# Performance work log

Hardware: AMD Instinct MI355X
Metric: run time of the kernel (lower is better)

Reference implementation:

```python
import jax, jax.numpy as jnp
import numpy as np

K_H, K_W = 3, 3
STRIDE, PAD = 1, 1
GN_GROUPS = 32
EPS = 1e-5


def setup_inputs() -> dict:
    key = jax.random.key(0)
    k1, k2, k3 = jax.random.split(key, 3)
    B, C, H, W = 4, 256, 64, 64
    Cout = 256
    x = jax.random.normal(k1, (B, C, H, W), jnp.float32)
    offset = jax.random.normal(k2, (B, 2 * K_H * K_W, H, W), jnp.float32)
    weight = jax.random.normal(k3, (Cout, C, K_H, K_W), jnp.float32) * 0.02
    gamma = jnp.ones((Cout,), jnp.float32)
    beta = jnp.zeros((Cout,), jnp.float32)
    return {"x": x, "offset": offset, "weight": weight, "gamma": gamma, "beta": beta}


def _deform_conv(x, offset, weight):
    B, C, H, W = x.shape
    Cout = weight.shape[0]
    K = K_H * K_W
    Ho = (H + 2 * PAD - K_H) // STRIDE + 1
    Wo = (W + 2 * PAD - K_W) // STRIDE + 1
    ky, kx = jnp.meshgrid(jnp.arange(K_H), jnp.arange(K_W), indexing='ij')
    ky = ky.reshape(K).astype(x.dtype)
    kx = kx.reshape(K).astype(x.dtype)
    # base sampling positions per kernel tap
    py_base = (jnp.arange(Ho) * STRIDE - PAD).astype(x.dtype)[None, :] + ky[:, None]  # [K,Ho]
    px_base = (jnp.arange(Wo) * STRIDE - PAD).astype(x.dtype)[None, :] + kx[:, None]  # [K,Wo]
    off = offset.reshape(B, K, 2, Ho, Wo)  # mmcv layout: (dy, dx) pairs per tap
    py = py_base[None, :, :, None] + off[:, :, 0]  # [B,K,Ho,Wo]
    px = px_base[None, :, None, :] + off[:, :, 1]  # [B,K,Ho,Wo]
    y0 = jnp.floor(py)
    x0 = jnp.floor(px)
    ly = py - y0
    lx = px - x0
    xf = x.reshape(B, C, H * W)

    def gather(yi, xi):
        valid = (yi >= 0) & (yi <= H - 1) & (xi >= 0) & (xi <= W - 1)
        yc = jnp.clip(yi, 0, H - 1).astype(jnp.int32)
        xc = jnp.clip(xi, 0, W - 1).astype(jnp.int32)
        idx = yc * W + xc  # [B,K,Ho,Wo]
        vals = jax.vmap(lambda xb, ib: xb[:, ib])(xf, idx)  # [B,C,K,Ho,Wo]
        return vals * valid[:, None].astype(x.dtype)

    g00 = gather(y0, x0)
    g01 = gather(y0, x0 + 1)
    g10 = gather(y0 + 1, x0)
    g11 = gather(y0 + 1, x0 + 1)
    wy = ly[:, None]  # [B,1,K,Ho,Wo]
    wx = lx[:, None]
    val = ((1 - wy) * (1 - wx) * g00 + (1 - wy) * wx * g01
           + wy * (1 - wx) * g10 + wy * wx * g11)  # [B,C,K,Ho,Wo]
    return jnp.einsum('bckhw,ock->bohw', val, weight.reshape(Cout, C, K))


def reference(x, offset, weight, gamma, beta):
    y = _deform_conv(x, offset, weight)  # [B,Cout,Ho,Wo]
    B, C, H, W = y.shape
    yg = y.reshape(B, GN_GROUPS, C // GN_GROUPS, H, W)
    mean = jnp.mean(yg, axis=(2, 3, 4), keepdims=True)
    var = jnp.var(yg, axis=(2, 3, 4), keepdims=True)
    yn = ((yg - mean) * jax.lax.rsqrt(var + EPS)).reshape(B, C, H, W)
    out = yn * gamma[None, :, None, None] + beta[None, :, None, None]
    return jax.nn.relu(out)
```

## Files before the change

### kernel.cpp

```cpp
#include <hip/hip_runtime.h>

typedef unsigned short ushort_t;
typedef __bf16 bf16x8 __attribute__((ext_vector_type(8)));
typedef float f32x4 __attribute__((ext_vector_type(4)));
typedef void __attribute__((address_space(1))) gvoid_t;
typedef void __attribute__((address_space(3))) lvoid_t;

__device__ __forceinline__ float bflo(unsigned u) { return __builtin_bit_cast(float, u << 16); }
__device__ __forceinline__ float bfhi(unsigned u) { return __builtin_bit_cast(float, u & 0xffff0000u); }
__device__ __forceinline__ unsigned f2bf_bits(float f) {
  unsigned u = __builtin_bit_cast(unsigned, f);
  return (u + 0x7fffu + ((u >> 16) & 1u)) >> 16;
}
__device__ __forceinline__ ushort_t f2bf(float f) { return (ushort_t)f2bf_bits(f); }

#define VMWAIT(N) asm volatile("s_waitcnt vmcnt(" #N ")" ::: "memory")
#define LGKM0 asm volatile("s_waitcnt lgkmcnt(0)" ::: "memory")

__global__ __launch_bounds__(256) void k_prep_w(const float* __restrict__ w,
                                                ushort_t* __restrict__ wb) {
  const int idx = blockIdx.x * 256 + threadIdx.x;
  const float* src = w + (size_t)idx * 9;
  #pragma unroll
  for (int k = 0; k < 9; ++k)
    wb[(k << 16) + idx] = f2bf(src[k]);
}

__global__ __launch_bounds__(256) void k_prep_x(const float* __restrict__ x,
                                                ushort_t* __restrict__ xt) {
  __shared__ ushort_t tile[64][68];
  const int bid = blockIdx.x;
  const int b = bid >> 8;
  const int ct = (bid >> 6) & 3;
  const int pt = bid & 63;
  const int t = threadIdx.x;
  const float* xb = x + ((size_t)(b * 256 + ct * 64)) * 4096 + pt * 64;
  #pragma unroll
  for (int i = 0; i < 16; ++i) {
    const int idx = t + 256 * i;
    const int c_l = idx >> 6, p_l = idx & 63;
    tile[c_l][p_l] = f2bf(xb[(size_t)c_l * 4096 + p_l]);
  }
  __syncthreads();
  ushort_t* xo = xt + ((size_t)(b * 4096 + pt * 64)) * 256 + ct * 64;
  #pragma unroll
  for (int i = 0; i < 16; ++i) {
    const int idx = t + 256 * i;
    const int p_l = idx >> 6, c_l = idx & 63;
    xo[(size_t)p_l * 256 + c_l] = tile[c_l][p_l];
  }
}

struct SMeta {
  float w00, w01, w10, w11;
  int i00, i01, i10, i11;
};
__device__ __forceinline__ SMeta meta_for(int h, int gw, int k, float oy, float ox) {
  SMeta m;
  const float py = (float)(h - 1 + k / 3) + oy;
  const float px = (float)(gw - 1 + k % 3) + ox;
  const float fy = floorf(py), fx = floorf(px);
  const float ly = py - fy, lx = px - fx;
  const int iy0 = (int)fy, ix0 = (int)fx;
  const float vy0 = (iy0 >= 0 && iy0 < 64) ? 1.f : 0.f;
  const float vy1 = (iy0 >= -1 && iy0 < 63) ? 1.f : 0.f;
  const float vx0 = (ix0 >= 0 && ix0 < 64) ? 1.f : 0.f;
  const float vx1 = (ix0 >= -1 && ix0 < 63) ? 1.f : 0.f;
  m.w00 = (1.f - ly) * (1.f - lx) * vy0 * vx0;
  m.w01 = (1.f - ly) * lx * vy0 * vx1;
  m.w10 = ly * (1.f - lx) * vy1 * vx0;
  m.w11 = ly * lx * vy1 * vx1;
  const int cy0 = min(max(iy0, 0), 63), cy1 = min(max(iy0 + 1, 0), 63);
  const int cx0 = min(max(ix0, 0), 63), cx1 = min(max(ix0 + 1, 0), 63);
  m.i00 = (cy0 * 64 + cx0) * 256;
  m.i01 = (cy0 * 64 + cx1) * 256;
  m.i10 = (cy1 * 64 + cx0) * 256;
  m.i11 = (cy1 * 64 + cx1) * 256;
  return m;
}

__device__ __forceinline__ unsigned lerp_pack(unsigned a, unsigned b, unsigned c, unsigned d,
                                              float w00, float w01, float w10, float w11) {
  float lo = w00 * bflo(a) + w01 * bflo(b) + w10 * bflo(c) + w11 * bflo(d);
  float hi = w00 * bfhi(a) + w01 * bfhi(b) + w10 * bfhi(c) + w11 * bfhi(d);
  return f2bf_bits(lo) | (f2bf_bits(hi) << 16);
}

__global__ __launch_bounds__(512) void k_gemm(const float* __restrict__ off,
                                              const ushort_t* __restrict__ xt,
                                              const ushort_t* __restrict__ wb,
                                              float* __restrict__ y,
                                              float* __restrict__ stats) {
  __shared__ __attribute__((aligned(16))) ushort_t Abuf[2][2][64 * 64];
  __shared__ __attribute__((aligned(16))) ushort_t Bbuf[2][2][256 * 64];

  const int bid = blockIdx.x;
  const int lb = ((bid & 7) << 5) | (bid >> 3);
  const int b = lb >> 6;
  const int h = lb & 63;
  const int t = threadIdx.x;
  const int wave = t >> 6;
  const int lane = t & 63;
  const int wq = lane >> 4;
  const int wr = lane & 15;
  const int wm = wave >> 2;
  const int wn = wave & 3;

  const int s_w = t >> 3;
  const int c8 = t & 7;

  const f32x4 zero = {0.f, 0.f, 0.f, 0.f};
  f32x4 acc[2][4];
  #pragma unroll
  for (int i = 0; i < 2; ++i)
    #pragma unroll
    for (int j = 0; j < 4; ++j) acc[i][j] = zero;

  const ushort_t* xtb = xt + (size_t)b * 4096 * 256;

  float oy[9], ox[9];
  {
    const float* offb = off + (size_t)b * 18 * 4096 + h * 64 + s_w;
    #pragma unroll
    for (int k = 0; k < 9; ++k) {
      oy[k] = offb[(2 * k) * 4096];
      ox[k] = offb[(2 * k + 1) * 4096];
    }
  }

  SMeta mg;
  uint4 qa00, qa01, qa10, qa11;
  uint4 qb00, qb01, qb10, qb11;

#define GATHER_ISSUE(TAP, C0)                             \
  {                                                       \
    mg = meta_for(h, s_w, (TAP), oy[(TAP)], ox[(TAP)]);   \
    const int cc = (C0) + c8 * 8;                         \
    qa00 = *(const uint4*)(xtb + mg.i00 + cc);            \
    qa01 = *(const uint4*)(xtb + mg.i01 + cc);            \
    qa10 = *(const uint4*)(xtb + mg.i10 + cc);            \
    qa11 = *(const uint4*)(xtb + mg.i11 + cc);            \
    qb00 = *(const uint4*)(xtb + mg.i00 + cc + 64);       \
    qb01 = *(const uint4*)(xtb + mg.i01 + cc + 64);       \
    qb10 = *(const uint4*)(xtb + mg.i10 + cc + 64);       \
    qb11 = *(const uint4*)(xtb + mg.i11 + cc + 64);       \
  }

#define B_ISSUE(TAP, C0, PB)                                                                   \
  {                                                                                            \
    _Pragma("unroll") for (int ch_ = 0; ch_ < 2; ++ch_) {                                      \
      _Pragma("unroll") for (int i_ = 0; i_ < 4; ++i_) {                                       \
        const int idx_ = i_ * 512 + t;                                                         \
        const int row_ = idx_ >> 3, slot_ = idx_ & 7;                                          \
        const ushort_t* g_ =                                                                   \
            wb + ((TAP) << 16) + row_ * 256 + (C0) + ch_ * 64 + ((slot_ ^ (row_ & 7)) << 3);   \
        __builtin_amdgcn_global_load_lds((gvoid_t*)g_,                                         \
                                         (lvoid_t*)((char*)&Bbuf[(PB)][ch_][0] + idx_ * 16),   \
                                         16, 0, 0);                                            \
      }                                                                                        \
    }                                                                                          \
  }

#define A_WRITE(PB)                                                                  \
  {                                                                                  \
    uint4 r;                                                                         \
    r.x = lerp_pack(qa00.x, qa01.x, qa10.x, qa11.x, mg.w00, mg.w01, mg.w10, mg.w11); \
    r.y = lerp_pack(qa00.y, qa01.y, qa10.y, qa11.y, mg.w00, mg.w01, mg.w10, mg.w11); \
    r.z = lerp_pack(qa00.z, qa01.z, qa10.z, qa11.z, mg.w00, mg.w01, mg.w10, mg.w11); \
    r.w = lerp_pack(qa00.w, qa01.w, qa10.w, qa11.w, mg.w00, mg.w01, mg.w10, mg.w11); \
    *(uint4*)&Abuf[(PB)][0][s_w * 64 + ((c8 ^ (s_w & 7)) << 3)] = r;                 \
    r.x = lerp_pack(qb00.x, qb01.x, qb10.x, qb11.x, mg.w00, mg.w01, mg.w10, mg.w11); \
    r.y = lerp_pack(qb00.y, qb01.y, qb10.y, qb11.y, mg.w00, mg.w01, mg.w10, mg.w11); \
    r.z = lerp_pack(qb00.z, qb01.z, qb10.z, qb11.z, mg.w00, mg.w01, mg.w10, mg.w11); \
    r.w = lerp_pack(qb00.w, qb01.w, qb10.w, qb11.w, mg.w00, mg.w01, mg.w10, mg.w11); \
    *(uint4*)&Abuf[(PB)][1][s_w * 64 + ((c8 ^ (s_w & 7)) << 3)] = r;                 \
  }

  {
    GATHER_ISSUE(0, 0);
    B_ISSUE(0, 0, 0);
    A_WRITE(0);
    GATHER_ISSUE(0, 128);
    VMWAIT(8);
    LGKM0;
    __builtin_amdgcn_s_barrier();
  }

  #pragma unroll
  for (int p = 0; p < 18; ++p) {
    const int pb = p & 1;
    const int nb = pb ^ 1;
    if (p < 17) {
      const int tap1 = (p + 1) >> 1;
      const int c01 = ((p + 1) & 1) << 7;
      B_ISSUE(tap1, c01, nb);
    }
    #pragma unroll
    for (int ks = 0; ks < 4; ++ks) {
      const int ch = ks >> 1;
      const int kk = ks & 1;
      bf16x8 af[2], bfr[4];
      #pragma unroll
      for (int tm = 0; tm < 2; ++tm) {
        const int row = wm * 32 + tm * 16 + wr;
        const int slot = (kk * 4 + wq) ^ (row & 7);
        af[tm] = *(const bf16x8*)&Abuf[pb][ch][row * 64 + slot * 8];
      }
      #pragma unroll
      for (int tn = 0; tn < 4; ++tn) {
        const int row = wn * 64 + tn * 16 + wr;
        const int slot = (kk * 4 + wq) ^ (row & 7);
        bfr[tn] = *(const bf16x8*)&Bbuf[pb][ch][row * 64 + slot * 8];
      }
      #pragma unroll
      for (int tm = 0; tm < 2; ++tm)
        #pragma unroll
        for (int tn = 0; tn < 4; ++tn)
          acc[tm][tn] =
              __builtin_amdgcn_mfma_f32_16x16x32_bf16(af[tm], bfr[tn], acc[tm][tn], 0, 0, 0);
    }
    if (p < 17) {
      A_WRITE(nb);
      if (p < 16) {
        const int tap2 = (p + 2) >> 1;
        const int c02 = ((p + 2) & 1) << 7;
        GATHER_ISSUE(tap2, c02);
        VMWAIT(8);
      } else {
        VMWAIT(0);
      }
      LGKM0;
      __builtin_amdgcn_s_barrier();
    }
  }
#undef GATHER_ISSUE
#undef B_ISSUE
#undef A_WRITE

  float* yb = y + ((size_t)(b * 4096 + h * 64)) * 256;
  #pragma unroll
  for (int tm = 0; tm < 2; ++tm) {
    #pragma unroll
    for (int tn = 0; tn < 4; ++tn) {
      const int o = wn * 64 + tn * 16 + wr;
      #pragma unroll
      for (int r2 = 0; r2 < 4; ++r2) {
        const int ww = wm * 32 + tm * 16 + wq * 4 + r2;
        yb[ww * 256 + o] = acc[tm][tn][r2];
      }
    }
  }
  #pragma unroll
  for (int tn = 0; tn < 4; ++tn) {
    float sum = 0.f, ss = 0.f;
    #pragma unroll
    for (int tm = 0; tm < 2; ++tm)
      #pragma unroll
      for (int r2 = 0; r2 < 4; ++r2) {
        const float v = acc[tm][tn][r2];
        sum += v;
        ss += v * v;
      }
    sum += __shfl_xor(sum, 16, 64);
    ss += __shfl_xor(ss, 16, 64);
    sum += __shfl_xor(sum, 32, 64);
    ss += __shfl_xor(ss, 32, 64);
    #pragma unroll
    for (int d = 1; d < 8; d <<= 1) {
      sum += __shfl_xor(sum, d, 64);
      ss += __shfl_xor(ss, d, 64);
    }
    if (wq == 0 && (wr & 7) == 0) {
      const int gi = wn * 8 + tn * 2 + (wr >> 3);
      atomicAdd(&stats[(b * 32 + gi) * 2], sum);
      atomicAdd(&stats[(b * 32 + gi) * 2 + 1], ss);
    }
  }
}

__global__ __launch_bounds__(256) void k_apply(const float* __restrict__ y,
                                               const float* __restrict__ stats,
                                               const float* __restrict__ gamma,
                                               const float* __restrict__ beta,
                                               float* __restrict__ out) {
  __shared__ float tile[64][65];
  __shared__ float sm[8], sr[8], sg[64], sb[64];
  const int bid = blockIdx.x;
  const int lb = ((bid & 7) << 7) | (bid >> 3);
  const int b = lb >> 8;
  const int st = (lb >> 2) & 63;
  const int ot = lb & 3;
  const int t = threadIdx.x;
  if (t < 8) {
    const int g = ot * 8 + t;
    const float s1 = stats[(b * 32 + g) * 2];
    const float s2 = stats[(b * 32 + g) * 2 + 1];
    const float mean = s1 * (1.f / 32768.f);
    const float var = s2 * (1.f / 32768.f) - mean * mean;
    sm[t] = mean;
    sr[t] = rsqrtf(var + 1e-5f);
  }
  if (t < 64) {
    sg[t] = gamma[ot * 64 + t];
    sb[t] = beta[ot * 64 + t];
  }
  const float* yb = y + ((size_t)(b * 4096 + st * 64)) * 256 + ot * 64;
  #pragma unroll
  for (int i = 0; i < 16; ++i) {
    const int idx = t + 256 * i;
    const int s_l = idx >> 6, o_l = idx & 63;
    tile[s_l][o_l] = yb[(size_t)s_l * 256 + o_l];
  }
  __syncthreads();
  float* ob = out + ((size_t)(b * 256 + ot * 64)) * 4096 + st * 64;
  #pragma unroll
  for (int i = 0; i < 16; ++i) {
    const int idx = t + 256 * i;
    const int o_l = idx >> 6, s_l = idx & 63;
    const int g = o_l >> 3;
    float v = (tile[s_l][o_l] - sm[g]) * sr[g] * sg[o_l] + sb[o_l];
    v = v > 0.f ? v : 0.f;
    ob[(size_t)o_l * 4096 + s_l] = v;
  }
}

extern "C" void kernel_launch(void* const* d_in, const int* in_sizes, int n_in,
                              void* d_out, int out_size, void* d_ws, size_t ws_size,
                              hipStream_t stream) {
  const float* x = (const float*)d_in[0];
  const float* off = (const float*)d_in[1];
  const float* w = (const float*)d_in[2];
  const float* gamma = (const float*)d_in[3];
  const float* beta = (const float*)d_in[4];
  float* out = (float*)d_out;

  char* ws = (char*)d_ws;
  float* y = (float*)(ws);
  ushort_t* xt = (ushort_t*)(ws + 16777216);
  ushort_t* wb = (ushort_t*)(ws + 25165824);
  float* stats = (float*)(ws + 26345472);

  hipMemsetAsync(stats, 0, 1024, stream);
  k_prep_w<<<256, 256, 0, stream>>>(w, wb);
  k_prep_x<<<1024, 256, 0, stream>>>(x, xt);
  k_gemm<<<256, 512, 0, stream>>>(off, xt, wb, y, stats);
  k_apply<<<1024, 256, 0, stream>>>(y, stats, gamma, beta, out);
}
```

Baseline: 83.74 us.

## Split GEMM block into producer and consumer waves with warp specialization

```diff
diff --git a/kernel.cpp b/kernel.cpp
--- a/kernel.cpp
+++ b/kernel.cpp
@@ -103,23 +103,23 @@
   const int lane = t & 63;
   const int wq = lane >> 4;
   const int wr = lane & 15;
-  const int wm = wave >> 2;
+  const bool prod = (wave >= 4);
   const int wn = wave & 3;
-
-  const int s_w = t >> 3;
-  const int c8 = t & 7;
+  const int pt = t & 255;
+  const int s_w = pt >> 2;
+  const int c4 = pt & 3;
 
   const f32x4 zero = {0.f, 0.f, 0.f, 0.f};
-  f32x4 acc[2][4];
-  #pragma unroll
-  for (int i = 0; i < 2; ++i)
+  f32x4 acc[4][4];
+  #pragma unroll
+  for (int i = 0; i < 4; ++i)
     #pragma unroll
     for (int j = 0; j < 4; ++j) acc[i][j] = zero;
 
   const ushort_t* xtb = xt + (size_t)b * 4096 * 256;
 
   float oy[9], ox[9];
-  {
+  if (prod) {
     const float* offb = off + (size_t)b * 18 * 4096 + h * 64 + s_w;
     #pragma unroll
     for (int k = 0; k < 9; ++k) {
@@ -128,152 +128,139 @@
     }
   }
 
-  SMeta mg;
-  uint4 qa00, qa01, qa10, qa11;
-  uint4 qb00, qb01, qb10, qb11;
-
-#define GATHER_ISSUE(TAP, C0)                             \
-  {                                                       \
-    mg = meta_for(h, s_w, (TAP), oy[(TAP)], ox[(TAP)]);   \
-    const int cc = (C0) + c8 * 8;                         \
-    qa00 = *(const uint4*)(xtb + mg.i00 + cc);            \
-    qa01 = *(const uint4*)(xtb + mg.i01 + cc);            \
-    qa10 = *(const uint4*)(xtb + mg.i10 + cc);            \
-    qa11 = *(const uint4*)(xtb + mg.i11 + cc);            \
-    qb00 = *(const uint4*)(xtb + mg.i00 + cc + 64);       \
-    qb01 = *(const uint4*)(xtb + mg.i01 + cc + 64);       \
-    qb10 = *(const uint4*)(xtb + mg.i10 + cc + 64);       \
-    qb11 = *(const uint4*)(xtb + mg.i11 + cc + 64);       \
-  }
-
-#define B_ISSUE(TAP, C0, PB)                                                                   \
+#define STAGE(TAP, C0, PB)                                                                     \
   {                                                                                            \
+    const SMeta m = meta_for(h, s_w, (TAP), oy[(TAP)], ox[(TAP)]);                             \
+    uint4 g[2][2][4];                                                                          \
     _Pragma("unroll") for (int ch_ = 0; ch_ < 2; ++ch_) {                                      \
-      _Pragma("unroll") for (int i_ = 0; i_ < 4; ++i_) {                                       \
-        const int idx_ = i_ * 512 + t;                                                         \
-        const int row_ = idx_ >> 3, slot_ = idx_ & 7;                                          \
-        const ushort_t* g_ =                                                                   \
-            wb + ((TAP) << 16) + row_ * 256 + (C0) + ch_ * 64 + ((slot_ ^ (row_ & 7)) << 3);   \
-        __builtin_amdgcn_global_load_lds((gvoid_t*)g_,                                         \
-                                         (lvoid_t*)((char*)&Bbuf[(PB)][ch_][0] + idx_ * 16),   \
-                                         16, 0, 0);                                            \
+      _Pragma("unroll") for (int sg_ = 0; sg_ < 2; ++sg_) {                                    \
+        const int cc_ = (C0) + ch_ * 64 + (c4 + sg_ * 4) * 8;                                  \
+        g[ch_][sg_][0] = *(const uint4*)(xtb + m.i00 + cc_);                                   \
+        g[ch_][sg_][1] = *(const uint4*)(xtb + m.i01 + cc_);                                   \
+        g[ch_][sg_][2] = *(const uint4*)(xtb + m.i10 + cc_);                                   \
+        g[ch_][sg_][3] = *(const uint4*)(xtb + m.i11 + cc_);                                   \
       }                                                                                        \
     }                                                                                          \
-  }
-
-#define A_WRITE(PB)                                                                  \
-  {                                                                                  \
-    uint4 r;                                                                         \
-    r.x = lerp_pack(qa00.x, qa01.x, qa10.x, qa11.x, mg.w00, mg.w01, mg.w10, mg.w11); \
-    r.y = lerp_pack(qa00.y, qa01.y, qa10.y, qa11.y, mg.w00, mg.w01, mg.w10, mg.w11); \
-    r.z = lerp_pack(qa00.z, qa01.z, qa10.z, qa11.z, mg.w00, mg.w01, mg.w10, mg.w11); \
-    r.w = lerp_pack(qa00.w, qa01.w, qa10.w, qa11.w, mg.w00, mg.w01, mg.w10, mg.w11); \
-    *(uint4*)&Abuf[(PB)][0][s_w * 64 + ((c8 ^ (s_w & 7)) << 3)] = r;                 \
-    r.x = lerp_pack(qb00.x, qb01.x, qb10.x, qb11.x, mg.w00, mg.w01, mg.w10, mg.w11); \
-    r.y = lerp_pack(qb00.y, qb01.y, qb10.y, qb11.y, mg.w00, mg.w01, mg.w10, mg.w11); \
-    r.z = lerp_pack(qb00.z, qb01.z, qb10.z, qb11.z, mg.w00, mg.w01, mg.w10, mg.w11); \
-    r.w = lerp_pack(qb00.w, qb01.w, qb10.w, qb11.w, mg.w00, mg.w01, mg.w10, mg.w11); \
-    *(uint4*)&Abuf[(PB)][1][s_w * 64 + ((c8 ^ (s_w & 7)) << 3)] = r;                 \
-  }
-
-  {
-    GATHER_ISSUE(0, 0);
-    B_ISSUE(0, 0, 0);
-    A_WRITE(0);
-    GATHER_ISSUE(0, 128);
-    VMWAIT(8);
-    LGKM0;
-    __builtin_amdgcn_s_barrier();
-  }
+    _Pragma("unroll") for (int i_ = 0; i_ < 16; ++i_) {                                        \
+      const int idx_ = i_ * 256 + pt;                            \
+      const int bch_ = idx_ >> 11;                                                  \
+      const int c_ = idx_ & 2047;                                                             \
+      const int row_ = c_ >> 3, slot_ = c_ & 7;                                               \
+      const ushort_t* g_ =                                                                     \
+          wb + ((TAP) << 16) + row_ * 256 + (C0) + bch_ * 64 + ((slot_ ^ (row_ & 7)) << 3);    \
+      __builtin_amdgcn_global_load_lds((gvoid_t*)g_,                                           \
+                                       (lvoid_t*)((char*)&Bbuf[(PB)][0][0] + idx_ * 16), 16,   \
+                                       0, 0);                                                  \
+    }                                                                                          \
+    _Pragma("unroll") for (int ch_ = 0; ch_ < 2; ++ch_) {                                      \
+      _Pragma("unroll") for (int sg_ = 0; sg_ < 2; ++sg_) {                                    \
+        uint4 r;                                                                               \
+        r.x = lerp_pack(g[ch_][sg_][0].x, g[ch_][sg_][1].x, g[ch_][sg_][2].x, g[ch_][sg_][3].x,\
+                        m.w00, m.w01, m.w10, m.w11);                                           \
+        r.y = lerp_pack(g[ch_][sg_][0].y, g[ch_][sg_][1].y, g[ch_][sg_][2].y, g[ch_][sg_][3].y,\
+                        m.w00, m.w01, m.w10, m.w11);                                           \
+        r.z = lerp_pack(g[ch_][sg_][0].z, g[ch_][sg_][1].z, g[ch_][sg_][2].z, g[ch_][sg_][3].z,\
+                        m.w00, m.w01, m.w10, m.w11);                                           \
+        r.w = lerp_pack(g[ch_][sg_][0].w, g[ch_][sg_][1].w, g[ch_][sg_][2].w, g[ch_][sg_][3].w,\
+                        m.w00, m.w01, m.w10, m.w11);                                           \
+        const int slice_ = c4 + sg_ * 4;                                                       \
+        *(uint4*)&Abuf[(PB)][ch_][s_w * 64 + ((slice_ ^ (s_w & 7)) << 3)] = r;                 \
+      }                                                                                        \
+    }                                                                                          \
+  }
+
+  if (prod) {
+    STAGE(0, 0, 0);
+    VMWAIT(0);
+  }
+  LGKM0;
+  __builtin_amdgcn_s_barrier();
 
   #pragma unroll
   for (int p = 0; p < 18; ++p) {
     const int pb = p & 1;
     const int nb = pb ^ 1;
+    if (prod) {
+      if (p < 17) {
+        const int tap1 = (p + 1) >> 1;
+        const int c01 = ((p + 1) & 1) << 7;
+        STAGE(tap1, c01, nb);
+        VMWAIT(0);
+      }
+    } else {
+      #pragma unroll
+      for (int ks = 0; ks < 4; ++ks) {
+        const int ch = ks >> 1;
+        const int kk = ks & 1;
+        bf16x8 af[4], bfr[4];
+        #pragma unroll
+        for (int tm = 0; tm < 4; ++tm) {
+          const int row = tm * 16 + wr;
+          const int slot = (kk * 4 + wq) ^ (row & 7);
+          af[tm] = *(const bf16x8*)&Abuf[pb][ch][row * 64 + slot * 8];
+        }
+        #pragma unroll
+        for (int tn = 0; tn < 4; ++tn) {
+          const int row = wn * 64 + tn * 16 + wr;
+          const int slot = (kk * 4 + wq) ^ (row & 7);
+          bfr[tn] = *(const bf16x8*)&Bbuf[pb][ch][row * 64 + slot * 8];
+        }
+        __builtin_amdgcn_s_setprio(1);
+        #pragma unroll
+        for (int tm = 0; tm < 4; ++tm)
+          #pragma unroll
+          for (int tn = 0; tn < 4; ++tn)
+            acc[tm][tn] =
+                __builtin_amdgcn_mfma_f32_16x16x32_bf16(af[tm], bfr[tn], acc[tm][tn], 0, 0, 0);
+        __builtin_amdgcn_s_setprio(0);
+      }
+    }
     if (p < 17) {
-      const int tap1 = (p + 1) >> 1;
-      const int c01 = ((p + 1) & 1) << 7;
-      B_ISSUE(tap1, c01, nb);
-    }
+      LGKM0;
+      __builtin_amdgcn_s_barrier();
+    }
+  }
+#undef STAGE
+
+  if (!prod) {
+    float* yb = y + ((size_t)(b * 4096 + h * 64)) * 256;
     #pragma unroll
-    for (int ks = 0; ks < 4; ++ks) {
-      const int ch = ks >> 1;
-      const int kk = ks & 1;
-      bf16x8 af[2], bfr[4];
-      #pragma unroll
-      for (int tm = 0; tm < 2; ++tm) {
-        const int row = wm * 32 + tm * 16 + wr;
-        const int slot = (kk * 4 + wq) ^ (row & 7);
-        af[tm] = *(const bf16x8*)&Abuf[pb][ch][row * 64 + slot * 8];
-      }
+    for (int tm = 0; tm < 4; ++tm) {
       #pragma unroll
       for (int tn = 0; tn < 4; ++tn) {
-        const int row = wn * 64 + tn * 16 + wr;
-        const int slot = (kk * 4 + wq) ^ (row & 7);
-        bfr[tn] = *(const bf16x8*)&Bbuf[pb][ch][row * 64 + slot * 8];
-      }
-      #pragma unroll
-      for (int tm = 0; tm < 2; ++tm)
-        #pragma unroll
-        for (int tn = 0; tn < 4; ++tn)
-          acc[tm][tn] =
-              __builtin_amdgcn_mfma_f32_16x16x32_bf16(af[tm], bfr[tn], acc[tm][tn], 0, 0, 0);
-    }
-    if (p < 17) {
-      A_WRITE(nb);
-      if (p < 16) {
-        const int tap2 = (p + 2) >> 1;
-        const int c02 = ((p + 2) & 1) << 7;
-        GATHER_ISSUE(tap2, c02);
-        VMWAIT(8);
-      } else {
-        VMWAIT(0);
-      }
-      LGKM0;
-      __builtin_amdgcn_s_barrier();
-    }
-  }
-#undef GATHER_ISSUE
-#undef B_ISSUE
-#undef A_WRITE
-
-  float* yb = y + ((size_t)(b * 4096 + h * 64)) * 256;
-  #pragma unroll
-  for (int tm = 0; tm < 2; ++tm) {
+        const int o = wn * 64 + tn * 16 + wr;
+        #pragma unroll
+        for (int r2 = 0; r2 < 4; ++r2) {
+          const int ww = tm * 16 + wq * 4 + r2;
+          yb[ww * 256 + o] = acc[tm][tn][r2];
+        }
+      }
+    }
     #pragma unroll
     for (int tn = 0; tn < 4; ++tn) {
-      const int o = wn * 64 + tn * 16 + wr;
+      float sum = 0.f, ss = 0.f;
       #pragma unroll
-      for (int r2 = 0; r2 < 4; ++r2) {
-        const int ww = wm * 32 + tm * 16 + wq * 4 + r2;
-        yb[ww * 256 + o] = acc[tm][tn][r2];
-      }
-    }
-  }
-  #pragma unroll
-  for (int tn = 0; tn < 4; ++tn) {
-    float sum = 0.f, ss = 0.f;
-    #pragma unroll
-    for (int tm = 0; tm < 2; ++tm)
+      for (int tm = 0; tm < 4; ++tm)
+        #pragma unroll
+        for (int r2 = 0; r2 < 4; ++r2) {
+          const float v = acc[tm][tn][r2];
+          sum += v;
+          ss += v * v;
+        }
+      sum += __shfl_xor(sum, 16, 64);
+      ss += __shfl_xor(ss, 16, 64);
+      sum += __shfl_xor(sum, 32, 64);
+      ss += __shfl_xor(ss, 32, 64);
       #pragma unroll
-      for (int r2 = 0; r2 < 4; ++r2) {
-        const float v = acc[tm][tn][r2];
-        sum += v;
-        ss += v * v;
-      }
-    sum += __shfl_xor(sum, 16, 64);
-    ss += __shfl_xor(ss, 16, 64);
-    sum += __shfl_xor(sum, 32, 64);
-    ss += __shfl_xor(ss, 32, 64);
-    #pragma unroll
-    for (int d = 1; d < 8; d <<= 1) {
-      sum += __shfl_xor(sum, d, 64);
-      ss += __shfl_xor(ss, d, 64);
-    }
-    if (wq == 0 && (wr & 7) == 0) {
-      const int gi = wn * 8 + tn * 2 + (wr >> 3);
-      atomicAdd(&stats[(b * 32 + gi) * 2], sum);
-      atomicAdd(&stats[(b * 32 + gi) * 2 + 1], ss);
+      for (int d = 1; d < 8; d <<= 1) {
+        sum += __shfl_xor(sum, d, 64);
+        ss += __shfl_xor(ss, d, 64);
+      }
+      if (wq == 0 && (wr & 7) == 0) {
+        const int gi = wn * 8 + tn * 2 + (wr >> 3);
+        atomicAdd(&stats[(b * 32 + gi) * 2], sum);
+        atomicAdd(&stats[(b * 32 + gi) * 2 + 1], ss);
+      }
     }
   }
 }
```

After: 86.01 us. 2.7% more time.
